# Kernel tuning notes

Measured on AMD Instinct MI355X. Metric: run time of the kernel, lower is better.

Reference implementation:

```python
import jax, jax.numpy as jnp
import numpy as np
import math

# ---------------- real Clebsch-Gordan machinery (numpy, built once at import) ----------------

def _fact(n):
    return math.factorial(n)

def _cg_complex(j1, m1, j2, m2, j3, m3):
    if m1 + m2 != m3:
        return 0.0
    pref = math.sqrt((2 * j3 + 1) * _fact(j3 + j1 - j2) * _fact(j3 - j1 + j2) * _fact(j1 + j2 - j3) / _fact(j1 + j2 + j3 + 1))
    pref *= math.sqrt(_fact(j3 + m3) * _fact(j3 - m3) * _fact(j1 - m1) * _fact(j1 + m1) * _fact(j2 - m2) * _fact(j2 + m2))
    s = 0.0
    for k in range(j1 + j2 - j3 + 1):
        d = [k, j1 + j2 - j3 - k, j1 - m1 - k, j2 + m2 - k, j3 - j2 + m1 + k, j3 - j1 - m2 + k]
        if min(d) < 0:
            continue
        s += (-1) ** k / math.prod(_fact(t) for t in d)
    return pref * s

def _real_U(l):
    # complex -> real spherical-harmonic change of basis, rows = real m (-l..l)
    U = np.zeros((2 * l + 1, 2 * l + 1), dtype=complex)
    U[l, l] = 1.0
    for m in range(1, l + 1):
        U[l + m, l + m] = (-1) ** m / math.sqrt(2)
        U[l + m, l - m] = 1.0 / math.sqrt(2)
        U[l - m, l + m] = -1j * (-1) ** m / math.sqrt(2)
        U[l - m, l - m] = 1j / math.sqrt(2)
    return U

def real_cg(l1, l2, l3):
    C = np.zeros((2 * l1 + 1, 2 * l2 + 1, 2 * l3 + 1), dtype=complex)
    for a in range(-l1, l1 + 1):
        for b in range(-l2, l2 + 1):
            for c in range(-l3, l3 + 1):
                C[a + l1, b + l2, c + l3] = _cg_complex(l1, a, l2, b, l3, c)
    T = np.einsum('ia,jb,kc,abc->ijk', _real_U(l1), _real_U(l2), _real_U(l3).conj(), C)
    Tr, Ti = T.real, T.imag
    T = Tr if np.abs(Tr).sum() >= np.abs(Ti).sum() else Ti
    return (T / np.linalg.norm(T)).astype(np.float32)

# ---------------- irreps / fully-connected tensor product ----------------

IR_SH = [(1, 0, 1), (1, 1, -1), (1, 2, 1), (1, 3, -1)]                      # 1x0e+1x1o+1x2e+1x3o (dim 16)
GATE_IN = [(16, 0, 1), (16, 0, -1), (8, 0, 1), (8, 0, -1), (8, 0, 1), (8, 0, -1), (16, 1, -1), (16, 1, 1)]  # dim 160
GATE_OUT = [(16, 0, 1), (16, 0, -1), (16, 1, -1), (16, 1, 1)]               # dim 128
IR_OUT = [(1, 0, 1)]                                                        # 1x0e

def ir_dim(irs):
    return sum(m * (2 * l + 1) for m, l, _ in irs)

def _slices(irs):
    out, off = [], 0
    for m, l, _ in irs:
        out.append((off, m, 2 * l + 1))
        off += m * (2 * l + 1)
    return out

def make_tp(ir1, ir2, ir3):
    s1, s2, s3 = _slices(ir1), _slices(ir2), _slices(ir3)
    insts, woff = [], 0
    for i1, (m1, l1, p1) in enumerate(ir1):
        for i2, (m2, l2, p2) in enumerate(ir2):
            for i3, (m3, l3, p3) in enumerate(ir3):
                if p1 * p2 == p3 and abs(l1 - l2) <= l3 <= l1 + l2:
                    insts.append((i1, i2, i3, woff))
                    woff += m1 * m2 * m3
    fan = {}
    for i1, i2, i3, _ in insts:
        fan[i3] = fan.get(i3, 0) + ir1[i1][0] * ir2[i2][0]
    paths = []
    for i1, i2, i3, w0 in insts:
        m1, l1, _ = ir1[i1]; m2, l2, _ = ir2[i2]; m3, l3, _ = ir3[i3]
        paths.append(dict(s1=s1[i1], s2=s2[i2], s3=s3[i3], w0=w0, nw=m1 * m2 * m3,
                          cg=jnp.asarray(real_cg(l1, l2, l3)),
                          alpha=math.sqrt((2 * l3 + 1) / fan[i3])))
    return dict(paths=paths, numel=woff, dim_out=ir_dim(ir3))

TP1 = make_tp(IR_SH, IR_SH, GATE_IN)     # weight_numel = 272
TP2 = make_tp(GATE_OUT, IR_SH, IR_OUT)   # weight_numel = 32

def tp_apply(tp, x1, x2, w):
    E = x1.shape[0]
    out = jnp.zeros((E, tp['dim_out']), x1.dtype)
    for p in tp['paths']:
        o1, m1, d1 = p['s1']; o2, m2, d2 = p['s2']; o3, m3, d3 = p['s3']
        a = x1[:, o1:o1 + m1 * d1].reshape(E, m1, d1)
        b = x2[:, o2:o2 + m2 * d2].reshape(E, m2, d2)
        ww = w[:, p['w0']:p['w0'] + p['nw']].reshape(E, m1, m2, m3)
        r = jnp.einsum('eui,evj,euvw,ijk->ewk', a, b, ww, p['cg']) * p['alpha']
        out = out.at[:, o3:o3 + m3 * d3].add(r.reshape(E, m3 * d3))
    return out

# ---------------- spherical harmonics (real, m=-l..l, component normalization) ----------------

SQ3, SQ5, SQ7 = math.sqrt(3), math.sqrt(5), math.sqrt(7)
SQ15, SQ42, SQ70, SQ105 = math.sqrt(15), math.sqrt(42), math.sqrt(70), math.sqrt(105)

def sph_harm_lmax3(v):
    x, y, z = v[:, 0], v[:, 1], v[:, 2]
    x2, y2, z2 = x * x, y * y, z * z
    sh0 = jnp.ones_like(x)[:, None]
    sh1 = SQ3 * jnp.stack([y, z, x], -1)
    sh2 = jnp.stack([SQ15 * x * y, SQ15 * y * z, 0.5 * SQ5 * (3 * z2 - 1), SQ15 * x * z, 0.5 * SQ15 * (x2 - y2)], -1)
    sh3 = jnp.stack([0.25 * SQ70 * y * (3 * x2 - y2), SQ105 * x * y * z, 0.25 * SQ42 * y * (5 * z2 - 1),
                     0.5 * SQ7 * z * (5 * z2 - 3), 0.25 * SQ42 * x * (5 * z2 - 1), 0.5 * SQ105 * z * (x2 - y2),
                     0.25 * SQ70 * x * (x2 - 3 * y2)], -1)
    return jnp.concatenate([sh0, sh1, sh2, sh3], -1)  # [E,16]

MAX_RADIUS, NUM_BASIS = 3.2, 10

def radial_embed(d):
    # soft_one_hot_linspace(basis='smooth_finite', cutoff=True) * sqrt(num_basis)
    step = MAX_RADIUS / (NUM_BASIS + 1)
    centers = jnp.linspace(0.0, MAX_RADIUS, NUM_BASIS + 2)[1:-1]
    u = (d[:, None] - centers) / step
    u2 = u * u
    inner = jnp.where(u2 < 1.0, u2 / jnp.maximum(1.0 - u2, 1e-6), 30.0)
    f = jnp.where(u2 < 1.0, 1.14136 * jnp.exp(-inner), 0.0)
    return f * math.sqrt(NUM_BASIS)

def fcnet(x, w1, w2):
    # e3nn FullyConnectedNet([10, 256, numel], relu): weight/sqrt(fan_in), relu normalized by sqrt(2)
    h = jax.nn.relu(x @ (w1 / math.sqrt(x.shape[1]))) * math.sqrt(2.0)
    return h @ (w2 / math.sqrt(w1.shape[1]))

def gate_act(x):
    # x: [N,160] = 16x0e | 16x0o | 8x0e | 8x0o | 8x0e | 8x0o | 16x1o | 16x1e
    s = jnp.concatenate([jax.nn.relu(x[:, :16]), jnp.tanh(x[:, 16:32])], -1)
    g = jnp.concatenate([jax.nn.relu(x[:, 32:40]), jnp.tanh(x[:, 40:48]),
                         jax.nn.relu(x[:, 48:56]), jnp.tanh(x[:, 56:64])], -1)  # [N,32]
    v = x[:, 64:].reshape(-1, 32, 3)  # 16x1o then 16x1e
    return jnp.concatenate([s, (v * g[:, :, None]).reshape(-1, 96)], -1)  # [N,128]

# ---------------- setup / reference ----------------

def setup_inputs():
    key = jax.random.key(0)
    ks = jax.random.split(key, 8)
    N, E, G = 20000, 640000, 16
    return {
        'pos': jax.random.normal(ks[0], (N, 3), jnp.float32),
        'w_fc1_1': jax.random.normal(ks[1], (NUM_BASIS, 256), jnp.float32),
        'w_fc1_2': jax.random.normal(ks[2], (256, TP1['numel']), jnp.float32),
        'w_fc2_1': jax.random.normal(ks[3], (NUM_BASIS, 256), jnp.float32),
        'w_fc2_2': jax.random.normal(ks[4], (256, TP2['numel']), jnp.float32),
        'edge_src': jax.random.randint(ks[5], (E,), 0, N, jnp.int32),
        'edge_dst': jax.random.randint(ks[6], (E,), 0, N, jnp.int32),
        'batch': jnp.sort(jax.random.randint(ks[7], (N,), 0, G, jnp.int32)),
        'num_graphs': G,
    }

def reference(pos, w_fc1_1, w_fc1_2, w_fc2_1, w_fc2_2, edge_src, edge_dst, batch, num_graphs):
    N = pos.shape[0]
    E = edge_src.shape[0]
    nn_norm = math.sqrt(E / N)  # num_neighbors ** 0.5
    ev = pos[edge_dst] - pos[edge_src]                       # [E,3]
    d = jnp.sqrt(jnp.sum(ev * ev, axis=1) + 1e-12)
    sh = sph_harm_lmax3(ev / d[:, None])                     # [E,16]
    emb = radial_embed(d)                                    # [E,10]
    x = jax.ops.segment_sum(sh, edge_dst, num_segments=N) / nn_norm
    # conv1: per-edge radial MLP -> CG tensor product -> scatter-add
    w = fcnet(emb, w_fc1_1, w_fc1_2)                         # [E,272]
    ef = tp_apply(TP1, x[edge_src], sh, w)                   # [E,160]
    x = jax.ops.segment_sum(ef, edge_dst, num_segments=N) / nn_norm
    x = gate_act(x)                                          # [N,128]
    # conv2
    w = fcnet(emb, w_fc2_1, w_fc2_2)                         # [E,32]
    ef = tp_apply(TP2, x[edge_src], sh, w)                   # [E,1]
    x = jax.ops.segment_sum(ef, edge_dst, num_segments=N) / nn_norm
    return jax.ops.segment_sum(x, batch, num_segments=num_graphs) / math.sqrt(N)  # [G,1]
```

## Files before the change

### kernel.cpp

```cpp
#include <hip/hip_runtime.h>
#include <cmath>
#include <cstdint>
#include <cstring>
#include <cstdlib>
#include <vector>
#include <algorithm>
#include <complex>

#define TILE 32

typedef __attribute__((ext_vector_type(8))) _Float16 f16x8;
typedef __attribute__((ext_vector_type(4))) float f32x4;

struct TPTables {
  uint32_t cg1p[40*10*2];
  uint32_t ovf[64*2];
  int novf;
  uint32_t tabA[12];
  uint32_t tabB[6];
  uint32_t tabC[3];
  uint32_t cg2p[32*4*2];
  uint32_t out2p[32];
  float alpha1[272];
  float alpha2[32];
};

static double factd(int n){ double r=1; for(int i=2;i<=n;i++) r*=(double)i; return r; }

static double cg_complex(int j1,int m1,int j2,int m2,int j3,int m3){
  if(m1+m2!=m3) return 0.0;
  double pref = std::sqrt((2*j3+1)*factd(j3+j1-j2)*factd(j3-j1+j2)*factd(j1+j2-j3)/factd(j1+j2+j3+1));
  pref *= std::sqrt(factd(j3+m3)*factd(j3-m3)*factd(j1-m1)*factd(j1+m1)*factd(j2-m2)*factd(j2+m2));
  double s=0.0;
  for(int k=0;k<=j1+j2-j3;k++){
    int dd[6] = {k, j1+j2-j3-k, j1-m1-k, j2+m2-k, j3-j2+m1+k, j3-j1-m2+k};
    bool ok=true; double prod=1.0;
    for(int t=0;t<6;t++){ if(dd[t]<0){ok=false;break;} prod*=factd(dd[t]); }
    if(!ok) continue;
    s += ((k&1)?-1.0:1.0)/prod;
  }
  return pref*s;
}

typedef std::complex<double> cd;
static void real_U(int l, cd* U){
  int n = 2*l+1;
  for(int i=0;i<n*n;i++) U[i]=cd(0,0);
  U[l*n+l] = cd(1,0);
  for(int m=1;m<=l;m++){
    double sgn = (m&1)? -1.0 : 1.0;
    double is2 = 1.0/std::sqrt(2.0);
    U[(l+m)*n + (l+m)] = cd(sgn*is2,0);
    U[(l+m)*n + (l-m)] = cd(is2,0);
    U[(l-m)*n + (l+m)] = cd(0,-sgn*is2);
    U[(l-m)*n + (l-m)] = cd(0,is2);
  }
}

static void real_cg_h(int l1,int l2,int l3, double* out){
  int n1=2*l1+1,n2=2*l2+1,n3=2*l3+1;
  std::vector<cd> C(n1*n2*n3);
  for(int a=-l1;a<=l1;a++)for(int b=-l2;b<=l2;b++)for(int c=-l3;c<=l3;c++)
    C[(size_t)((a+l1)*n2+(b+l2))*n3+(c+l3)] = cd(cg_complex(l1,a,l2,b,l3,c),0);
  std::vector<cd> U1(n1*n1),U2(n2*n2),U3(n3*n3);
  real_U(l1,U1.data()); real_U(l2,U2.data()); real_U(l3,U3.data());
  std::vector<cd> T((size_t)n1*n2*n3, cd(0,0));
  for(int i=0;i<n1;i++)for(int j=0;j<n2;j++)for(int k=0;k<n3;k++){
    cd acc(0,0);
    for(int a=0;a<n1;a++){ cd u1=U1[i*n1+a]; if(u1==cd(0,0)) continue;
      for(int b=0;b<n2;b++){ cd u2=U2[j*n2+b]; if(u2==cd(0,0)) continue;
        for(int c=0;c<n3;c++){ cd u3=std::conj(U3[k*n3+c]); if(u3==cd(0,0)) continue;
          acc += u1*u2*u3*C[(size_t)(a*n2+b)*n3+c];
        } } }
    T[(size_t)(i*n2+j)*n3+k]=acc;
  }
  double sr=0, si=0;
  for(auto&z:T){ sr += std::fabs(z.real()); si += std::fabs(z.imag()); }
  int tot=n1*n2*n3;
  std::vector<double> R(tot);
  for(int i=0;i<tot;i++) R[i] = (sr>=si)? T[i].real() : T[i].imag();
  double nrm=0; for(double v:R) nrm += v*v; nrm = std::sqrt(nrm);
  for(int i=0;i<tot;i++) out[i] = R[i]/nrm;
}

struct HIrr{int m,l,p;};
static int map_id(int i){return i;}
static int map_gate(int i){return (i<16)? i : i-16;}

static void build_one(const std::vector<HIrr>& ir1, const std::vector<HIrr>& ir2,
                      const std::vector<HIrr>& ir3, int (*map1)(int),
                      std::vector<uint32_t>& cg_pk, std::vector<float>& cg_c,
                      std::vector<uint32_t>& out_pk, std::vector<float>& out_c)
{
  int n1=(int)ir1.size(), n2=(int)ir2.size(), n3=(int)ir3.size();
  std::vector<int> s1(n1), s2(n2), s3(n3);
  { int o=0; for(int i=0;i<n1;i++){ s1[i]=o; o+=ir1[i].m*(2*ir1[i].l+1);} }
  { int o=0; for(int i=0;i<n2;i++){ s2[i]=o; o+=ir2[i].m*(2*ir2[i].l+1);} }
  { int o=0; for(int i=0;i<n3;i++){ s3[i]=o; o+=ir3[i].m*(2*ir3[i].l+1);} }
  struct Inst{int i1,i2,i3,w0;};
  std::vector<Inst> insts; int woff=0;
  for(int i1=0;i1<n1;i1++)for(int i2=0;i2<n2;i2++)for(int i3=0;i3<n3;i3++){
    const HIrr&A=ir1[i1];const HIrr&B=ir2[i2];const HIrr&C=ir3[i3];
    int dl = A.l-B.l; if(dl<0) dl=-dl;
    if(A.p*B.p==C.p && dl<=C.l && C.l<=A.l+B.l){
      insts.push_back({i1,i2,i3,woff}); woff += A.m*B.m*C.m;
    }
  }
  std::vector<int> fan(n3,0);
  for(auto&P:insts) fan[P.i3] += ir1[P.i1].m*ir2[P.i2].m;
  int sbase=0;
  for(auto&P:insts){
    const HIrr&A=ir1[P.i1];const HIrr&B=ir2[P.i2];const HIrr&C=ir3[P.i3];
    int d1=2*A.l+1,d2=2*B.l+1,d3=2*C.l+1;
    double cg[343];
    real_cg_h(A.l,B.l,C.l,cg);
    double alpha = std::sqrt((double)d3/(double)fan[P.i3]);
    for(int u=0;u<A.m;u++)for(int v=0;v<B.m;v++){
      for(int k=0;k<d3;k++)
        for(int i=0;i<d1;i++)for(int j=0;j<d2;j++){
          double c = cg[(i*d2+j)*d3+k];
          if(std::fabs(c)<1e-8) continue;
          int iabs = map1(s1[P.i1]+u*d1+i);
          int jabs = s2[P.i2]+v*d2+j;
          cg_pk.push_back((uint32_t)iabs | ((uint32_t)jabs<<8) | ((uint32_t)(sbase+k)<<16));
          cg_c.push_back((float)c);
        }
      for(int w=0;w<C.m;w++)for(int k=0;k<d3;k++){
        out_pk.push_back((uint32_t)(s3[P.i3]+w*d3+k) | ((uint32_t)(P.w0+(u*B.m+v)*C.m+w)<<8) | ((uint32_t)(sbase+k)<<20));
        out_c.push_back((float)alpha);
      }
      sbase += d3;
    }
  }
}

static uint32_t fbits(float f){ uint32_t u; memcpy(&u,&f,4); return u; }

static void build_tables(TPTables& T){
  std::vector<HIrr> IR_SH   ={{1,0,1},{1,1,-1},{1,2,1},{1,3,-1}};
  std::vector<HIrr> GATE_IN ={{16,0,1},{16,0,-1},{8,0,1},{8,0,-1},{8,0,1},{8,0,-1},{16,1,-1},{16,1,1}};
  std::vector<HIrr> GATE_OUT={{16,0,1},{16,0,-1},{16,1,-1},{16,1,1}};
  std::vector<HIrr> IR_OUT  ={{1,0,1}};
  std::vector<uint32_t> cg1,o1,cg2,o2; std::vector<float> cg1c,o1c,cg2c,o2c;
  build_one(IR_SH,IR_SH,GATE_IN,map_id,cg1,cg1c,o1,o1c);
  build_one(GATE_OUT,IR_SH,IR_OUT,map_gate,cg2,cg2c,o2,o2c);
  memset(&T,0,sizeof(T));
  {
    int cnt[40]; memset(cnt,0,sizeof(cnt));
    for(size_t idx=0; idx<cg1.size(); ++idx){
      int i = cg1[idx]&0xff, j=(cg1[idx]>>8)&0xff, s=(int)(cg1[idx]>>16);
      uint32_t pidx = (uint32_t)(i*16+j);
      if(s<40 && cnt[s]<10){
        T.cg1p[(s*10+cnt[s])*2]   = pidx;
        T.cg1p[(s*10+cnt[s])*2+1] = fbits(cg1c[idx]);
        cnt[s]++;
      } else if(T.novf<64){
        T.ovf[T.novf*2]   = pidx | ((uint32_t)s<<8);
        T.ovf[T.novf*2+1] = fbits(cg1c[idx]);
        T.novf++;
      }
    }
  }
  {
    int GIl[8]={0,0,0,0,0,0,1,1}, GIp[8]={1,-1,1,-1,1,-1,-1,1}, GIm[8]={16,16,8,8,8,8,16,16};
    int SHl[4]={0,1,2,3}, SHp[4]={1,-1,1,-1};
    int w0=0, sb=0, nA0=0,nA1=0,nA2=0,nB=0,nC=0;
    for(int i1=0;i1<4;i1++)for(int i2=0;i2<4;i2++)for(int i3=0;i3<8;i3++){
      int dl=SHl[i1]-SHl[i2]; if(dl<0) dl=-dl;
      if(SHp[i1]*SHp[i2]==GIp[i3] && dl<=GIl[i3] && GIl[i3]<=SHl[i1]+SHl[i2]){
        uint32_t ent = (uint32_t)w0 | ((uint32_t)sb<<16);
        if(i3==0 && nA0<4) T.tabA[nA0++] = ent;
        else if(i3==2 && nA1<4) T.tabA[4+nA1++] = ent;
        else if(i3==4 && nA2<4) T.tabA[8+nA2++] = ent;
        else if(i3==6 && nB<6) T.tabB[nB++] = ent;
        else if(i3==7 && nC<3) T.tabC[nC++] = ent;
        w0 += GIm[i3];
        sb += 2*GIl[i3]+1;
      }
    }
  }
  for(size_t idx=0; idx<o1.size(); ++idx){
    int widx = (o1[idx]>>8)&0xfff;
    if(widx<272) T.alpha1[widx] = o1c[idx];
  }
  {
    int cnt[32]; memset(cnt,0,sizeof(cnt));
    for(size_t idx=0; idx<cg2.size(); ++idx){
      int s = (int)(cg2[idx]>>16);
      if(s<32 && cnt[s]<4){
        T.cg2p[(s*4+cnt[s])*2]   = cg2[idx]&0xFFFF;
        T.cg2p[(s*4+cnt[s])*2+1] = fbits(cg2c[idx]);
        cnt[s]++;
      }
    }
  }
  for(size_t idx=0; idx<o2.size() && idx<32; ++idx){
    int widx = (o2[idx]>>8)&0xfff;
    int s    = (int)(o2[idx]>>20);
    T.out2p[idx] = (uint32_t)widx | ((uint32_t)s<<16);
    if(widx<32) T.alpha2[widx] = o2c[idx];
  }
}

__device__ __forceinline__ unsigned short f2h(float f){
  _Float16 h = (_Float16)f;
  unsigned short u; __builtin_memcpy(&u, &h, 2); return u;
}
__device__ __forceinline__ float h2f(unsigned short u){
  _Float16 h; __builtin_memcpy(&h, &u, 2); return (float)h;
}

__device__ __forceinline__ void sph16(float x,float y,float z,float* sh){
  float x2=x*x, y2=y*y, z2=z*z;
  const float SQ3=1.7320508075688772f, SQ5=2.23606797749979f, SQ7=2.6457513110645907f;
  const float SQ15=3.872983346207417f, SQ42=6.48074069840786f, SQ70=8.366600265340756f, SQ105=10.246950765959598f;
  sh[0]=1.f;
  sh[1]=SQ3*y;  sh[2]=SQ3*z;  sh[3]=SQ3*x;
  sh[4]=SQ15*x*y; sh[5]=SQ15*y*z; sh[6]=0.5f*SQ5*(3.f*z2-1.f); sh[7]=SQ15*x*z; sh[8]=0.5f*SQ15*(x2-y2);
  sh[9]=0.25f*SQ70*y*(3.f*x2-y2); sh[10]=SQ105*x*y*z; sh[11]=0.25f*SQ42*y*(5.f*z2-1.f);
  sh[12]=0.5f*SQ7*z*(5.f*z2-3.f); sh[13]=0.25f*SQ42*x*(5.f*z2-1.f);
  sh[14]=0.5f*SQ105*z*(x2-y2);    sh[15]=0.25f*SQ70*x*(x2-3.f*y2);
}

__device__ __forceinline__ void radial10(float d, float* emb){
  const float step = 0.2909090909090909f;
  #pragma unroll
  for(int b=0;b<10;b++){
    float c = step*(float)(b+1);
    float u = (d-c)/step;
    float u2 = u*u;
    float f = 0.f;
    if(u2<1.f) f = 1.14136f*__expf(-u2/fmaxf(1.f-u2,1e-6f));
    emb[b] = f*3.1622776601683795f;
  }
}

__global__ void k_zero(float* a, size_t na, float* b, size_t nb, float* c, size_t nc,
                       int* d, size_t nd){
  size_t total = na+nb+nc+nd;
  for(size_t i = (size_t)blockIdx.x*blockDim.x+threadIdx.x; i<total; i += (size_t)gridDim.x*blockDim.x){
    if(i<na) a[i]=0.f;
    else if(i<na+nb) b[i-na]=0.f;
    else if(i<na+nb+nc) c[i-na-nb]=0.f;
    else d[i-na-nb-nc]=0;
  }
}

__global__ void k_deg(const int* __restrict__ edst, int* __restrict__ deg, int E){
  int e = blockIdx.x*256 + threadIdx.x;
  if(e<E) atomicAdd(&deg[edst[e]], 1);
}

__global__ __launch_bounds__(1024) void k_scan(const int* __restrict__ deg, int* __restrict__ row,
                                               int* __restrict__ cursor, int N){
  __shared__ int buf[2][1024];
  __shared__ int carry;
  int t = threadIdx.x;
  if(t==0) carry=0;
  __syncthreads();
  for(int base=0; base<N; base+=1024){
    int i = base+t;
    int v = (i<N)? deg[i] : 0;
    int cur=0;
    buf[0][t]=v; __syncthreads();
    for(int off=1; off<1024; off<<=1){
      int val = buf[cur][t];
      if(t>=off) val += buf[cur][t-off];
      buf[cur^1][t]=val; __syncthreads();
      cur^=1;
    }
    if(i<N) row[i] = carry + buf[cur][t] - v;
    int tot = buf[cur][1023];
    __syncthreads();
    if(t==0) carry += tot;
    __syncthreads();
  }
  if(t==0) row[N]=carry;
  for(int i=t;i<N;i+=1024) cursor[i]=0;
}

__global__ void k_fill(const int* __restrict__ edst, const int* __restrict__ row,
                       int* __restrict__ cursor, int* __restrict__ perm, int E){
  int e = blockIdx.x*256 + threadIdx.x;
  if(e<E){
    int d = edst[e];
    int p = atomicAdd(&cursor[d], 1);
    perm[row[d]+p] = e;
  }
}

#define NB1 (17*8*64*8)
#define NB2 (2*8*64*8)
#define NW1 (16*64*8)
__global__ void k_prep(const float* __restrict__ W2a, const float* __restrict__ W2b,
                       const float* __restrict__ W1a, const float* __restrict__ W1b,
                       unsigned short* __restrict__ B1, unsigned short* __restrict__ B2,
                       unsigned short* __restrict__ W1p1, unsigned short* __restrict__ W1p2,
                       const TPTables* __restrict__ T){
  int i = blockIdx.x*256 + threadIdx.x;
  if(i < NB1){
    int s = i&7, lane = (i>>3)&63, ks = (i>>9)&7, ct = i>>12;
    int g = lane>>4;
    int k = ks*32 + g*4 + (s&3) + ((s>>2)<<4);
    int c = ct*16 + (lane&15);
    B1[i] = f2h(W2a[k*272+c]*0.0625f*T->alpha1[c]);
  } else if(i < NB1+NB2){
    int j = i - NB1;
    int s = j&7, lane = (j>>3)&63, ks = (j>>9)&7, ct = j>>12;
    int g = lane>>4;
    int k = ks*32 + g*4 + (s&3) + ((s>>2)<<4);
    int c = ct*16 + (lane&15);
    B2[j] = f2h(W2b[k*32+c]*0.0625f*T->alpha2[c]);
  } else if(i < NB1+NB2+NW1){
    int j = i - NB1 - NB2;
    int s = j&7, lane = (j>>3)&63, ct = j>>9;
    int g = lane>>4;
    int k = g*4 + (s&3) + ((s>>2)<<4);
    int c = ct*16 + (lane&15);
    W1p1[j] = (k<10)? f2h(W1a[k*256+c]*0.4472135954999579f) : (unsigned short)0;
  } else if(i < NB1+NB2+2*NW1){
    int j = i - NB1 - NB2 - NW1;
    int s = j&7, lane = (j>>3)&63, ct = j>>9;
    int g = lane>>4;
    int k = g*4 + (s&3) + ((s>>2)<<4);
    int c = ct*16 + (lane&15);
    W1p2[j] = (k<10)? f2h(W1b[k*256+c]*0.4472135954999579f) : (unsigned short)0;
  }
}

__global__ __launch_bounds__(256) void k_edge_pre(
    const float* __restrict__ pos, const int* __restrict__ esrc, const int* __restrict__ edst,
    const int* __restrict__ perm, float* __restrict__ x, int E){
  __shared__ float shs[256*17];
  __shared__ int dsts[256];
  int t = threadIdx.x;
  int idx = blockIdx.x*256 + t;
  int d = -1;
  if(idx<E){
    int e = perm[idx];
    int s = esrc[e]; d = edst[e];
    float ex=pos[3*d]-pos[3*s], ey=pos[3*d+1]-pos[3*s+1], ez=pos[3*d+2]-pos[3*s+2];
    float dd = sqrtf(ex*ex+ey*ey+ez*ez+1e-12f);
    sph16(ex/dd, ey/dd, ez/dd, &shs[t*17]);
  }
  dsts[t] = d;
  __syncthreads();
  bool leader = (d>=0) && (t==0 || dsts[t-1]!=d);
  if(leader){
    int len=1;
    while(t+len<256 && dsts[t+len]==d) len++;
    #pragma unroll
    for(int j=0;j<16;j++){
      float a=0.f;
      for(int k=0;k<len;k++) a += shs[(t+k)*17+j];
      atomicAdd(&x[(size_t)d*16+j], a);
    }
  }
}

#define F1_WT 1632
#define F1_AF 5984
#define F1_S  10208
#define F1_EF 10848
#define F1_TOT 12928

__global__ __launch_bounds__(512,6) void k_fc1_tp1(
    const float* __restrict__ pos, const int* __restrict__ esrc, const int* __restrict__ edst,
    const int* __restrict__ perm,
    const unsigned short* __restrict__ W1p, const unsigned short* __restrict__ B1,
    const float* __restrict__ xnode, float* __restrict__ ef1,
    const TPTables* __restrict__ T, int E, float inv_nn)
{
  __shared__ __align__(16) float sm[F1_TOT];
  __shared__ int src_t[TILE], dst_t[TILE];
  float* sh_t  = sm;
  float* x1_t  = sm + 544;
  float* emb_t = sm + 1088;
  unsigned short* Wt_h = (unsigned short*)(sm + F1_WT);
  unsigned short* AFh  = (unsigned short*)(sm + F1_AF);
  unsigned short* S16h = (unsigned short*)(sm + F1_S);
  float* ef_h = sm + F1_EF;
  int t = threadIdx.x;
  int e0 = blockIdx.x*TILE;
  int nE = min(TILE, E-e0);
  int e = t>>4, g = t&15, w = t>>6, lane = t&63;
  int g2 = lane>>4, lr = lane&15;

  if(t<TILE){
    float embr[10];
    if(t<nE){
      int e2 = perm[e0+t];
      int s=esrc[e2], d=edst[e2];
      src_t[t]=s; dst_t[t]=d;
      float ex=pos[3*d]-pos[3*s], ey=pos[3*d+1]-pos[3*s+1], ez=pos[3*d+2]-pos[3*s+2];
      float dd=sqrtf(ex*ex+ey*ey+ez*ez+1e-12f);
      sph16(ex/dd,ey/dd,ez/dd, &sh_t[t*17]);
      radial10(dd, embr);
    } else {
      src_t[t]=0; dst_t[t]=-1;
      #pragma unroll
      for(int j=0;j<16;j++) sh_t[t*17+j]=0.f;
      #pragma unroll
      for(int b=0;b<10;b++) embr[b]=0.f;
    }
    #pragma unroll
    for(int b=0;b<10;b++) emb_t[t*17+b]=embr[b];
  }
  __syncthreads();
  x1_t[e*17+g] = xnode[(size_t)src_t[e]*16+g]*inv_nn;
  {
    float af0[8], af1[8];
    #pragma unroll
    for(int s=0;s<8;s++){
      int k = g2*4 + (s&3) + ((s>>2)<<4);
      af0[s] = (k<10)? emb_t[lr*17+k] : 0.f;
      af1[s] = (k<10)? emb_t[(16+lr)*17+k] : 0.f;
    }
    union { f16x8 v; uint32_t w4[4]; } a0u, a1u;
    #pragma unroll
    for(int i=0;i<4;i++){
      a0u.w4[i] = (uint32_t)f2h(af0[2*i]) | ((uint32_t)f2h(af0[2*i+1])<<16);
      a1u.w4[i] = (uint32_t)f2h(af1[2*i]) | ((uint32_t)f2h(af1[2*i+1])<<16);
    }
    #pragma unroll
    for(int q=0;q<2;q++){
      int ct = w*2+q;
      f16x8 b = *(const f16x8*)(W1p + ((size_t)(ct*64+lane))*8);
      f32x4 z = {0.f,0.f,0.f,0.f};
      f32x4 c0 = __builtin_amdgcn_mfma_f32_16x16x32_f16(a0u.v, b, z, 0,0,0);
      f32x4 c1 = __builtin_amdgcn_mfma_f32_16x16x32_f16(a1u.v, b, z, 0,0,0);
      int ks = ct>>1, sp = (lr&3)|((ct&1)<<2);
      #pragma unroll
      for(int r=0;r<4;r++){
        int lnp = ((lr>>2)<<4) + (g2<<2) + r;
        AFh[(ks*64+lnp)*8+sp]     = f2h(fmaxf(c0[r],0.f));
        AFh[((8+ks)*64+lnp)*8+sp] = f2h(fmaxf(c1[r],0.f));
      }
    }
  }
  __syncthreads();
  {
    for(int ct=w; ct<17; ct+=8){
      f32x4 acc0 = {0.f,0.f,0.f,0.f}, acc1 = {0.f,0.f,0.f,0.f};
      #pragma unroll
      for(int ks=0;ks<8;ks++){
        f16x8 b  = *(const f16x8*)(B1 + ((size_t)(ct*8+ks)*64 + lane)*8);
        f16x8 a0 = *(const f16x8*)(AFh + (ks*64+lane)*8);
        f16x8 a1 = *(const f16x8*)(AFh + ((8+ks)*64+lane)*8);
        acc0 = __builtin_amdgcn_mfma_f32_16x16x32_f16(a0, b, acc0, 0,0,0);
        acc1 = __builtin_amdgcn_mfma_f32_16x16x32_f16(a1, b, acc1, 0,0,0);
      }
      #pragma unroll
      for(int r=0;r<4;r++){
        Wt_h[(g2*4+r)*272 + ct*16+lr]    = f2h(acc0[r]);
        Wt_h[(16+g2*4+r)*272 + ct*16+lr] = f2h(acc1[r]);
      }
    }
  }
  __syncthreads();
  {
    float xv = x1_t[e*17+g];
    float shv[16];
    #pragma unroll
    for(int j=0;j<16;j++) shv[j]=sh_t[e*17+j];
    uint32_t* dst = (uint32_t*)AFh + e*132 + g*8;
    #pragma unroll
    for(int jp=0;jp<8;jp++)
      dst[jp] = (uint32_t)f2h(xv*shv[2*jp]) | ((uint32_t)f2h(xv*shv[2*jp+1])<<16);
  }
  __syncthreads();
  {
    const uint2* cgt = (const uint2*)T->cg1p;
    #pragma unroll
    for(int p=0;p<3;p++){
      int slot = p*16+g;
      if(slot<39){
        float acc=0.f;
        #pragma unroll
        for(int q=0;q<10;q++){
          uint2 v = cgt[slot*10+q];
          acc += __uint_as_float(v.y) * h2f(AFh[e*264 + (v.x&0xff)]);
        }
        S16h[e*40+slot] = f2h(acc);
      }
    }
  }
  __syncthreads();
  if(t<TILE){
    int n = T->novf;
    for(int o=0;o<n;o++){
      uint2 v = ((const uint2*)T->ovf)[o];
      int slot = (v.x>>8)&0xff;
      S16h[t*40+slot] = f2h(h2f(S16h[t*40+slot]) + __uint_as_float(v.y)*h2f(AFh[t*264+(v.x&0xff)]));
    }
  }
  __syncthreads();
  float a0=0.f, a1=0.f, accB[3]={0.f,0.f,0.f}, accC[3]={0.f,0.f,0.f};
  {
    int grp = (g>=8)+(g>=12);
    int base = (grp==0)?0:((grp==1)?16:24);
    int ol = g*2 - base;
    #pragma unroll
    for(int p=0;p<4;p++){
      uint32_t v = T->tabA[grp*4+p];
      int w0 = v&0xffff, sb = v>>16;
      float Sv = h2f(S16h[e*40+sb]);
      uint32_t wp = *(const uint32_t*)(Wt_h + e*272 + w0 + ol);
      a0 += h2f((unsigned short)(wp&0xffff))*Sv;
      a1 += h2f((unsigned short)(wp>>16))*Sv;
    }
    #pragma unroll
    for(int p=0;p<6;p++){
      uint32_t v = T->tabB[p];
      int w0 = v&0xffff, sb = v>>16;
      float Wv = h2f(Wt_h[e*272 + w0 + g]);
      accB[0] += Wv*h2f(S16h[e*40+sb]);
      accB[1] += Wv*h2f(S16h[e*40+sb+1]);
      accB[2] += Wv*h2f(S16h[e*40+sb+2]);
    }
    #pragma unroll
    for(int p=0;p<3;p++){
      uint32_t v = T->tabC[p];
      int w0 = v&0xffff, sb = v>>16;
      float Wv = h2f(Wt_h[e*272 + w0 + g]);
      accC[0] += Wv*h2f(S16h[e*40+sb]);
      accC[1] += Wv*h2f(S16h[e*40+sb+1]);
      accC[2] += Wv*h2f(S16h[e*40+sb+2]);
    }
  }
  #pragma unroll
  for(int h=0; h<2; h++){
    for(int i=t;i<TILE*65;i+=512) ef_h[i]=0.f;
    __syncthreads();
    if(h==0){
      ef_h[e*65 + g*2]   = a0;
      ef_h[e*65 + g*2+1] = a1;
      #pragma unroll
      for(int k=0;k<3;k++){
        int b = g*3+k;
        if(b<32) ef_h[e*65 + 32+b] = accB[k];
      }
    } else {
      #pragma unroll
      for(int k=0;k<3;k++){
        int b = g*3+k;
        if(b>=32) ef_h[e*65 + (b-32)] = accB[k];
      }
      #pragma unroll
      for(int k=0;k<3;k++)
        ef_h[e*65 + 16 + g*3+k] = accC[k];
    }
    __syncthreads();
    if(t<64){
      int rank = h*64+t;
      int opos = rank<16? rank : rank<24? rank+16 : rank<32? rank+24 : rank+32;
      float acc=0.f;
      for(int e2=0;e2<TILE;e2++){
        int d = dst_t[e2];
        if(d>=0) acc += ef_h[e2*65+t];
        bool bnd = (e2==TILE-1) || (dst_t[e2+1]!=d);
        if(bnd){
          if(d>=0 && acc!=0.f) atomicAdd(&ef1[(size_t)d*160 + opos], acc);
          acc=0.f;
        }
      }
    }
    __syncthreads();
  }
}

__global__ void k_gate(const float* __restrict__ ef1, float* __restrict__ xg, int N, float inv_nn){
  int n = blockIdx.x*256+threadIdx.x;
  if(n>=N) return;
  const float* v = ef1 + (size_t)n*160;
  float* o = xg + (size_t)n*128;
  float g[32];
  #pragma unroll
  for(int i=0;i<16;i++) o[i] = fmaxf(v[i]*inv_nn, 0.f);
  #pragma unroll
  for(int i=0;i<16;i++) o[16+i] = tanhf(v[16+i]*inv_nn);
  #pragma unroll
  for(int i=0;i<8;i++) g[i]    = fmaxf(v[32+i]*inv_nn,0.f);
  #pragma unroll
  for(int i=0;i<8;i++) g[8+i]  = tanhf(v[40+i]*inv_nn);
  #pragma unroll
  for(int i=0;i<8;i++) g[16+i] = fmaxf(v[48+i]*inv_nn,0.f);
  #pragma unroll
  for(int i=0;i<8;i++) g[24+i] = tanhf(v[56+i]*inv_nn);
  #pragma unroll
  for(int u=0;u<32;u++){
    float gu = g[u];
    #pragma unroll
    for(int k=0;k<3;k++) o[32+u*3+k] = v[64+u*3+k]*inv_nn*gu;
  }
}

#define F2_WT 3168
#define F2_AF 4320
#define F2_BINS 8416
#define F2_TOT 8432

__global__ __launch_bounds__(512,6) void k_fc2_tp2(
    const float* __restrict__ pos, const int* __restrict__ esrc, const int* __restrict__ edst,
    const int* __restrict__ perm, const int* __restrict__ batch,
    const unsigned short* __restrict__ W1p, const unsigned short* __restrict__ B2,
    const float* __restrict__ xg, float* __restrict__ out,
    const TPTables* __restrict__ T, int E, float out_scale, int G)
{
  __shared__ __align__(16) float sm[F2_TOT];
  __shared__ int src_t[TILE], dst_t[TILE], g_t[TILE];
  float* sh_t  = sm;
  float* emb_t = sm + 544;
  float* xg_t  = sm + 1088;
  float* Wt    = sm + F2_WT;
  unsigned short* AFh = (unsigned short*)(sm + F2_AF);
  float* S_l  = sm + F2_AF;
  float* bins = sm + F2_BINS;
  int t = threadIdx.x;
  int e0 = blockIdx.x*TILE;
  int nE = min(TILE, E-e0);
  int e = t>>4, g = t&15, w = t>>6, lane = t&63;
  int g2 = lane>>4, lr = lane&15;

  if(t<TILE){
    float embr[10];
    if(t<nE){
      int e2 = perm[e0+t];
      int s=esrc[e2], d=edst[e2];
      src_t[t]=s; dst_t[t]=d; g_t[t]=batch[d];
      float ex=pos[3*d]-pos[3*s], ey=pos[3*d+1]-pos[3*s+1], ez=pos[3*d+2]-pos[3*s+2];
      float dd=sqrtf(ex*ex+ey*ey+ez*ez+1e-12f);
      sph16(ex/dd,ey/dd,ez/dd, &sh_t[t*17]);
      radial10(dd, embr);
    } else {
      src_t[t]=0; dst_t[t]=-1; g_t[t]=0;
      #pragma unroll
      for(int j=0;j<16;j++) sh_t[t*17+j]=0.f;
      #pragma unroll
      for(int b=0;b<10;b++) embr[b]=0.f;
    }
    #pragma unroll
    for(int b=0;b<10;b++) emb_t[t*17+b]=embr[b];
  } else if(t<TILE+16){
    bins[t-TILE]=0.f;
  }
  __syncthreads();
  #pragma unroll
  for(int rep=0;rep<4;rep++){
    int j = g + rep*16;
    xg_t[e*65+j] = xg[(size_t)src_t[e]*128 + (j<16? j : j+16)];
  }
  {
    float af0[8], af1[8];
    #pragma unroll
    for(int s=0;s<8;s++){
      int k = g2*4 + (s&3) + ((s>>2)<<4);
      af0[s] = (k<10)? emb_t[lr*17+k] : 0.f;
      af1[s] = (k<10)? emb_t[(16+lr)*17+k] : 0.f;
    }
    union { f16x8 v; uint32_t w4[4]; } a0u, a1u;
    #pragma unroll
    for(int i=0;i<4;i++){
      a0u.w4[i] = (uint32_t)f2h(af0[2*i]) | ((uint32_t)f2h(af0[2*i+1])<<16);
      a1u.w4[i] = (uint32_t)f2h(af1[2*i]) | ((uint32_t)f2h(af1[2*i+1])<<16);
    }
    #pragma unroll
    for(int q=0;q<2;q++){
      int ct = w*2+q;
      f16x8 b = *(const f16x8*)(W1p + ((size_t)(ct*64+lane))*8);
      f32x4 z = {0.f,0.f,0.f,0.f};
      f32x4 c0 = __builtin_amdgcn_mfma_f32_16x16x32_f16(a0u.v, b, z, 0,0,0);
      f32x4 c1 = __builtin_amdgcn_mfma_f32_16x16x32_f16(a1u.v, b, z, 0,0,0);
      int ks = ct>>1, sp = (lr&3)|((ct&1)<<2);
      #pragma unroll
      for(int r=0;r<4;r++){
        int lnp = ((lr>>2)<<4) + (g2<<2) + r;
        AFh[(ks*64+lnp)*8+sp]     = f2h(fmaxf(c0[r],0.f));
        AFh[((8+ks)*64+lnp)*8+sp] = f2h(fmaxf(c1[r],0.f));
      }
    }
  }
  __syncthreads();
  {
    if(w<2){
      int ct = w;
      f32x4 acc0 = {0.f,0.f,0.f,0.f}, acc1 = {0.f,0.f,0.f,0.f};
      #pragma unroll
      for(int ks=0;ks<8;ks++){
        f16x8 b  = *(const f16x8*)(B2 + ((size_t)(ct*8+ks)*64 + lane)*8);
        f16x8 a0 = *(const f16x8*)(AFh + (ks*64+lane)*8);
        f16x8 a1 = *(const f16x8*)(AFh + ((8+ks)*64+lane)*8);
        acc0 = __builtin_amdgcn_mfma_f32_16x16x32_f16(a0, b, acc0, 0,0,0);
        acc1 = __builtin_amdgcn_mfma_f32_16x16x32_f16(a1, b, acc1, 0,0,0);
      }
      #pragma unroll
      for(int r=0;r<4;r++){
        Wt[(g2*4+r)*36 + ct*16+lr]    = acc0[r];
        Wt[(16+g2*4+r)*36 + ct*16+lr] = acc1[r];
      }
    }
  }
  __syncthreads();
  {
    const uint2* cgt = (const uint2*)T->cg2p;
    #pragma unroll
    for(int p=0;p<2;p++){
      int slot = p*16 + g;
      float acc=0.f;
      #pragma unroll
      for(int q=0;q<4;q++){
        uint2 v = cgt[slot*4+q];
        acc += __uint_as_float(v.y) * xg_t[e*65+(v.x&0xff)] * sh_t[e*17+((v.x>>8)&0xff)];
      }
      S_l[e*33+slot]=acc;
    }
  }
  __syncthreads();
  {
    uint32_t u0 = T->out2p[2*g], u1 = T->out2p[2*g+1];
    float v = Wt[e*36+(u0&0xffff)] * S_l[e*33+(u0>>16)]
            + Wt[e*36+(u1&0xffff)] * S_l[e*33+(u1>>16)];
    #pragma unroll
    for(int m=1;m<16;m<<=1) v += __shfl_xor(v, m, 64);
    if(g==0 && e<nE) atomicAdd(&bins[g_t[e]], v);
  }
  __syncthreads();
  if(t<G) atomicAdd(&out[t], bins[t]*out_scale);
}

extern "C" void kernel_launch(void* const* d_in, const int* in_sizes, int n_in,
                              void* d_out, int out_size, void* d_ws, size_t ws_size,
                              hipStream_t stream) {
  const float* pos  = (const float*)d_in[0];
  const float* w11  = (const float*)d_in[1];
  const float* w12  = (const float*)d_in[2];
  const float* w21  = (const float*)d_in[3];
  const float* w22  = (const float*)d_in[4];
  const int*   esrc = (const int*)d_in[5];
  const int*   edst = (const int*)d_in[6];
  const int*   batch= (const int*)d_in[7];
  int E = in_sizes[5];
  int N = in_sizes[0]/3;
  int G = out_size;

  double nn = std::sqrt((double)E/(double)N);
  float inv_nn    = (float)(1.0/nn);
  float out_scale = (float)(1.0/(nn*std::sqrt((double)N)));

  float* ws = (float*)d_ws;
  float* x   = ws;
  float* ef1 = x   + (size_t)N*16;
  float* xg  = ef1 + (size_t)N*160;
  TPTables* dT = (TPTables*)(xg + (size_t)N*128);
  unsigned short* B1   = (unsigned short*)(((char*)dT) + ((sizeof(TPTables)+255)&~(size_t)255));
  unsigned short* B2   = B1 + NB1;
  unsigned short* W1p1 = B2 + NB2;
  unsigned short* W1p2 = W1p1 + NW1;
  int* deg    = (int*)(W1p2 + NW1);
  int* row    = deg + N;
  int* cursor = row + (N+1);
  int* perm   = cursor + N;

  static TPTables hT;
  build_tables(hT);
  hipMemcpyAsync(dT, &hT, sizeof(TPTables), hipMemcpyHostToDevice, stream);

  size_t nz = (size_t)N*16 + (size_t)N*160 + G + N;
  int zgrid = (int)((nz+255)/256); if(zgrid>2048) zgrid=2048;
  k_zero<<<zgrid,256,0,stream>>>(x, (size_t)N*16, ef1, (size_t)N*160, (float*)d_out, (size_t)G, deg, (size_t)N);
  k_deg<<<(E+255)/256,256,0,stream>>>(edst, deg, E);
  k_scan<<<1,1024,0,stream>>>(deg, row, cursor, N);
  k_fill<<<(E+255)/256,256,0,stream>>>(edst, row, cursor, perm, E);
  k_prep<<<(NB1+NB2+2*NW1+255)/256,256,0,stream>>>(w12, w22, w11, w21, B1, B2, W1p1, W1p2, dT);
  k_edge_pre<<<(E+255)/256,256,0,stream>>>(pos, esrc, edst, perm, x, E);
  k_fc1_tp1<<<(E+TILE-1)/TILE,512,0,stream>>>(pos, esrc, edst, perm, W1p1, B1, x, ef1, dT, E, inv_nn);
  k_gate<<<(N+255)/256,256,0,stream>>>(ef1, xg, N, inv_nn);
  k_fc2_tp2<<<(E+TILE-1)/TILE,512,0,stream>>>(pos, esrc, edst, perm, batch, W1p2, B2, xg,
                                              (float*)d_out, dT, E, out_scale, G);
}
```

Baseline: 938.3 us.

## Swizzle LDS layouts, pad strides, and drop overflow CG pass in fused kernels

Applies a lane swizzle to the fp16 activation tile written after the first MFMA layer and read by the second, and pads the per-edge weight row strides (272 to 276 halves, 36 to 37 floats) to cut LDS bank conflicts. It widens the per-slot CG table from 10 to 16 entries so every term fits in one pass, which removes the serial overflow loop and a barrier. It also drops the per-half zeroing of the ef buffer and its barrier. The wider CG loop adds some zero-padded multiply-adds, and removing the zeroing assumes every ef entry gets overwritten.

```diff
diff --git a/kernel.cpp b/kernel.cpp
--- a/kernel.cpp
+++ b/kernel.cpp
@@ -13,9 +13,7 @@
 typedef __attribute__((ext_vector_type(4))) float f32x4;
 
 struct TPTables {
-  uint32_t cg1p[40*10*2];
-  uint32_t ovf[64*2];
-  int novf;
+  uint32_t cg1p[40*16*2];
   uint32_t tabA[12];
   uint32_t tabB[6];
   uint32_t tabC[3];
@@ -150,14 +148,10 @@
     for(size_t idx=0; idx<cg1.size(); ++idx){
       int i = cg1[idx]&0xff, j=(cg1[idx]>>8)&0xff, s=(int)(cg1[idx]>>16);
       uint32_t pidx = (uint32_t)(i*16+j);
-      if(s<40 && cnt[s]<10){
-        T.cg1p[(s*10+cnt[s])*2]   = pidx;
-        T.cg1p[(s*10+cnt[s])*2+1] = fbits(cg1c[idx]);
+      if(s<40 && cnt[s]<16){
+        T.cg1p[(s*16+cnt[s])*2]   = pidx;
+        T.cg1p[(s*16+cnt[s])*2+1] = fbits(cg1c[idx]);
         cnt[s]++;
-      } else if(T.novf<64){
-        T.ovf[T.novf*2]   = pidx | ((uint32_t)s<<8);
-        T.ovf[T.novf*2+1] = fbits(cg1c[idx]);
-        T.novf++;
       }
     }
   }
@@ -209,6 +203,7 @@
 __device__ __forceinline__ float h2f(unsigned short u){
   _Float16 h; __builtin_memcpy(&h, &u, 2); return (float)h;
 }
+__device__ __forceinline__ int sig(int x){ return ((x&3)<<4) | (x>>2); }
 
 __device__ __forceinline__ void sph16(float x,float y,float z,float* sh){
   float x2=x*x, y2=y*y, z2=z*z;
@@ -359,10 +354,11 @@
 }
 
 #define F1_WT 1632
-#define F1_AF 5984
-#define F1_S  10208
-#define F1_EF 10848
-#define F1_TOT 12928
+#define F1_AF 6048
+#define F1_S  10272
+#define F1_EF 10912
+#define F1_TOT 12992
+#define WST 276
 
 __global__ __launch_bounds__(512,6) void k_fc1_tp1(
     const float* __restrict__ pos, const int* __restrict__ esrc, const int* __restrict__ edst,
@@ -433,27 +429,29 @@
       #pragma unroll
       for(int r=0;r<4;r++){
         int lnp = ((lr>>2)<<4) + (g2<<2) + r;
-        AFh[(ks*64+lnp)*8+sp]     = f2h(fmaxf(c0[r],0.f));
-        AFh[((8+ks)*64+lnp)*8+sp] = f2h(fmaxf(c1[r],0.f));
-      }
-    }
-  }
-  __syncthreads();
-  {
+        int sl = sig(lnp);
+        AFh[(ks*64+sl)*8+sp]     = f2h(fmaxf(c0[r],0.f));
+        AFh[((8+ks)*64+sl)*8+sp] = f2h(fmaxf(c1[r],0.f));
+      }
+    }
+  }
+  __syncthreads();
+  {
+    int sl = sig(lane);
     for(int ct=w; ct<17; ct+=8){
       f32x4 acc0 = {0.f,0.f,0.f,0.f}, acc1 = {0.f,0.f,0.f,0.f};
       #pragma unroll
       for(int ks=0;ks<8;ks++){
         f16x8 b  = *(const f16x8*)(B1 + ((size_t)(ct*8+ks)*64 + lane)*8);
-        f16x8 a0 = *(const f16x8*)(AFh + (ks*64+lane)*8);
-        f16x8 a1 = *(const f16x8*)(AFh + ((8+ks)*64+lane)*8);
+        f16x8 a0 = *(const f16x8*)(AFh + (ks*64+sl)*8);
+        f16x8 a1 = *(const f16x8*)(AFh + ((8+ks)*64+sl)*8);
         acc0 = __builtin_amdgcn_mfma_f32_16x16x32_f16(a0, b, acc0, 0,0,0);
         acc1 = __builtin_amdgcn_mfma_f32_16x16x32_f16(a1, b, acc1, 0,0,0);
       }
       #pragma unroll
       for(int r=0;r<4;r++){
-        Wt_h[(g2*4+r)*272 + ct*16+lr]    = f2h(acc0[r]);
-        Wt_h[(16+g2*4+r)*272 + ct*16+lr] = f2h(acc1[r]);
+        Wt_h[(g2*4+r)*WST + ct*16+lr]    = f2h(acc0[r]);
+        Wt_h[(16+g2*4+r)*WST + ct*16+lr] = f2h(acc1[r]);
       }
     }
   }
@@ -474,24 +472,15 @@
     #pragma unroll
     for(int p=0;p<3;p++){
       int slot = p*16+g;
-      if(slot<39){
+      if(slot<40){
         float acc=0.f;
         #pragma unroll
-        for(int q=0;q<10;q++){
-          uint2 v = cgt[slot*10+q];
+        for(int q=0;q<16;q++){
+          uint2 v = cgt[slot*16+q];
           acc += __uint_as_float(v.y) * h2f(AFh[e*264 + (v.x&0xff)]);
         }
         S16h[e*40+slot] = f2h(acc);
       }
-    }
-  }
-  __syncthreads();
-  if(t<TILE){
-    int n = T->novf;
-    for(int o=0;o<n;o++){
-      uint2 v = ((const uint2*)T->ovf)[o];
-      int slot = (v.x>>8)&0xff;
-      S16h[t*40+slot] = f2h(h2f(S16h[t*40+slot]) + __uint_as_float(v.y)*h2f(AFh[t*264+(v.x&0xff)]));
     }
   }
   __syncthreads();
@@ -505,7 +494,7 @@
       uint32_t v = T->tabA[grp*4+p];
       int w0 = v&0xffff, sb = v>>16;
       float Sv = h2f(S16h[e*40+sb]);
-      uint32_t wp = *(const uint32_t*)(Wt_h + e*272 + w0 + ol);
+      uint32_t wp = *(const uint32_t*)(Wt_h + e*WST + w0 + ol);
       a0 += h2f((unsigned short)(wp&0xffff))*Sv;
       a1 += h2f((unsigned short)(wp>>16))*Sv;
     }
@@ -513,7 +502,7 @@
     for(int p=0;p<6;p++){
       uint32_t v = T->tabB[p];
       int w0 = v&0xffff, sb = v>>16;
-      float Wv = h2f(Wt_h[e*272 + w0 + g]);
+      float Wv = h2f(Wt_h[e*WST + w0 + g]);
       accB[0] += Wv*h2f(S16h[e*40+sb]);
       accB[1] += Wv*h2f(S16h[e*40+sb+1]);
       accB[2] += Wv*h2f(S16h[e*40+sb+2]);
@@ -522,7 +511,7 @@
     for(int p=0;p<3;p++){
       uint32_t v = T->tabC[p];
       int w0 = v&0xffff, sb = v>>16;
-      float Wv = h2f(Wt_h[e*272 + w0 + g]);
+      float Wv = h2f(Wt_h[e*WST + w0 + g]);
       accC[0] += Wv*h2f(S16h[e*40+sb]);
       accC[1] += Wv*h2f(S16h[e*40+sb+1]);
       accC[2] += Wv*h2f(S16h[e*40+sb+2]);
@@ -530,8 +519,6 @@
   }
   #pragma unroll
   for(int h=0; h<2; h++){
-    for(int i=t;i<TILE*65;i+=512) ef_h[i]=0.f;
-    __syncthreads();
     if(h==0){
       ef_h[e*65 + g*2]   = a0;
       ef_h[e*65 + g*2+1] = a1;
@@ -596,9 +583,9 @@
 }
 
 #define F2_WT 3168
-#define F2_AF 4320
-#define F2_BINS 8416
-#define F2_TOT 8432
+#define F2_AF 4352
+#define F2_BINS 8448
+#define F2_TOT 8464
 
 __global__ __launch_bounds__(512,6) void k_fc2_tp2(
     const float* __restrict__ pos, const int* __restrict__ esrc, const int* __restrict__ edst,
@@ -675,8 +662,9 @@
       #pragma unroll
       for(int r=0;r<4;r++){
         int lnp = ((lr>>2)<<4) + (g2<<2) + r;
-        AFh[(ks*64+lnp)*8+sp]     = f2h(fmaxf(c0[r],0.f));
-        AFh[((8+ks)*64+lnp)*8+sp] = f2h(fmaxf(c1[r],0.f));
+        int sl = sig(lnp);
+        AFh[(ks*64+sl)*8+sp]     = f2h(fmaxf(c0[r],0.f));
+        AFh[((8+ks)*64+sl)*8+sp] = f2h(fmaxf(c1[r],0.f));
       }
     }
   }
@@ -684,19 +672,20 @@
   {
     if(w<2){
       int ct = w;
+      int sl = sig(lane);
       f32x4 acc0 = {0.f,0.f,0.f,0.f}, acc1 = {0.f,0.f,0.f,0.f};
       #pragma unroll
       for(int ks=0;ks<8;ks++){
         f16x8 b  = *(const f16x8*)(B2 + ((size_t)(ct*8+ks)*64 + lane)*8);
-        f16x8 a0 = *(const f16x8*)(AFh + (ks*64+lane)*8);
-        f16x8 a1 = *(const f16x8*)(AFh + ((8+ks)*64+lane)*8);
+        f16x8 a0 = *(const f16x8*)(AFh + (ks*64+sl)*8);
+        f16x8 a1 = *(const f16x8*)(AFh + ((8+ks)*64+sl)*8);
         acc0 = __builtin_amdgcn_mfma_f32_16x16x32_f16(a0, b, acc0, 0,0,0);
         acc1 = __builtin_amdgcn_mfma_f32_16x16x32_f16(a1, b, acc1, 0,0,0);
       }
       #pragma unroll
       for(int r=0;r<4;r++){
-        Wt[(g2*4+r)*36 + ct*16+lr]    = acc0[r];
-        Wt[(16+g2*4+r)*36 + ct*16+lr] = acc1[r];
+        Wt[(g2*4+r)*37 + ct*16+lr]    = acc0[r];
+        Wt[(16+g2*4+r)*37 + ct*16+lr] = acc1[r];
       }
     }
   }
@@ -718,8 +707,8 @@
   __syncthreads();
   {
     uint32_t u0 = T->out2p[2*g], u1 = T->out2p[2*g+1];
-    float v = Wt[e*36+(u0&0xffff)] * S_l[e*33+(u0>>16)]
-            + Wt[e*36+(u1&0xffff)] * S_l[e*33+(u1>>16)];
+    float v = Wt[e*37+(u0&0xffff)] * S_l[e*33+(u0>>16)]
+            + Wt[e*37+(u1&0xffff)] * S_l[e*33+(u1>>16)];
     #pragma unroll
     for(int m=1;m<16;m<<=1) v += __shfl_xor(v, m, 64);
     if(g==0 && e<nE) atomicAdd(&bins[g_t[e]], v);
```

After: 1.140 ms. 21.5% more time.

## Parallelize CSR prefix scan across blocks and swizzle LDS MFMA operand layout

Applied to the files above, without the earlier changes.

Replaces the single-block serial-chunked prefix scan over node degrees with a three-kernel multi-block scan: per-block scans, a wavefront scan of block sums, then an offset add. This removes a long single-workgroup serial loop. It also XOR-swizzles the LDS row index for the hidden-activation fp16 buffer in both fc+TP kernels to reduce bank conflicts on stores and MFMA operand loads. The scan handles at most 64 blocks (N up to 65536) and adds two extra launches.

```diff
diff --git a/kernel.cpp b/kernel.cpp
--- a/kernel.cpp
+++ b/kernel.cpp
@@ -209,6 +209,7 @@
 __device__ __forceinline__ float h2f(unsigned short u){
   _Float16 h; __builtin_memcpy(&h, &u, 2); return (float)h;
 }
+__device__ __forceinline__ int sig(int x){ return x ^ (x>>3); }
 
 __device__ __forceinline__ void sph16(float x,float y,float z,float* sh){
   float x2=x*x, y2=y*y, z2=z*z;
@@ -251,32 +252,42 @@
   if(e<E) atomicAdd(&deg[edst[e]], 1);
 }
 
-__global__ __launch_bounds__(1024) void k_scan(const int* __restrict__ deg, int* __restrict__ row,
-                                               int* __restrict__ cursor, int N){
+__global__ __launch_bounds__(1024) void k_scan1(const int* __restrict__ deg, int* __restrict__ row,
+                                                int* __restrict__ bsum, int N){
   __shared__ int buf[2][1024];
-  __shared__ int carry;
   int t = threadIdx.x;
-  if(t==0) carry=0;
-  __syncthreads();
-  for(int base=0; base<N; base+=1024){
-    int i = base+t;
-    int v = (i<N)? deg[i] : 0;
-    int cur=0;
-    buf[0][t]=v; __syncthreads();
-    for(int off=1; off<1024; off<<=1){
-      int val = buf[cur][t];
-      if(t>=off) val += buf[cur][t-off];
-      buf[cur^1][t]=val; __syncthreads();
-      cur^=1;
-    }
-    if(i<N) row[i] = carry + buf[cur][t] - v;
-    int tot = buf[cur][1023];
-    __syncthreads();
-    if(t==0) carry += tot;
-    __syncthreads();
-  }
-  if(t==0) row[N]=carry;
-  for(int i=t;i<N;i+=1024) cursor[i]=0;
+  int i = blockIdx.x*1024 + t;
+  int v = (i<N)? deg[i] : 0;
+  int cur=0;
+  buf[0][t]=v; __syncthreads();
+  for(int off=1; off<1024; off<<=1){
+    int val = buf[cur][t];
+    if(t>=off) val += buf[cur][t-off];
+    buf[cur^1][t]=val; __syncthreads();
+    cur^=1;
+  }
+  if(i<N) row[i] = buf[cur][t] - v;
+  if(t==1023) bsum[blockIdx.x] = buf[cur][t];
+}
+__global__ void k_scan2(int* __restrict__ bsum, int nb){
+  int t = threadIdx.x;
+  int v = (t<nb)? bsum[t] : 0;
+  #pragma unroll
+  for(int off=1; off<64; off<<=1){
+    int u = __shfl_up(v, off, 64);
+    if(t>=off) v += u;
+  }
+  if(t<nb) bsum[t] = v;
+}
+__global__ void k_scan3(int* __restrict__ row, const int* __restrict__ bsum,
+                        int* __restrict__ cursor, int N, int nb){
+  int i = blockIdx.x*256 + threadIdx.x;
+  if(i<N){
+    int b = i>>10;
+    if(b>0) row[i] += bsum[b-1];
+    cursor[i]=0;
+  }
+  if(i==0) row[N] = bsum[nb-1];
 }
 
 __global__ void k_fill(const int* __restrict__ edst, const int* __restrict__ row,
@@ -433,20 +444,22 @@
       #pragma unroll
       for(int r=0;r<4;r++){
         int lnp = ((lr>>2)<<4) + (g2<<2) + r;
-        AFh[(ks*64+lnp)*8+sp]     = f2h(fmaxf(c0[r],0.f));
-        AFh[((8+ks)*64+lnp)*8+sp] = f2h(fmaxf(c1[r],0.f));
-      }
-    }
-  }
-  __syncthreads();
-  {
+        int sl = sig(lnp);
+        AFh[(ks*64+sl)*8+sp]     = f2h(fmaxf(c0[r],0.f));
+        AFh[((8+ks)*64+sl)*8+sp] = f2h(fmaxf(c1[r],0.f));
+      }
+    }
+  }
+  __syncthreads();
+  {
+    int sl = sig(lane);
     for(int ct=w; ct<17; ct+=8){
       f32x4 acc0 = {0.f,0.f,0.f,0.f}, acc1 = {0.f,0.f,0.f,0.f};
       #pragma unroll
       for(int ks=0;ks<8;ks++){
         f16x8 b  = *(const f16x8*)(B1 + ((size_t)(ct*8+ks)*64 + lane)*8);
-        f16x8 a0 = *(const f16x8*)(AFh + (ks*64+lane)*8);
-        f16x8 a1 = *(const f16x8*)(AFh + ((8+ks)*64+lane)*8);
+        f16x8 a0 = *(const f16x8*)(AFh + (ks*64+sl)*8);
+        f16x8 a1 = *(const f16x8*)(AFh + ((8+ks)*64+sl)*8);
         acc0 = __builtin_amdgcn_mfma_f32_16x16x32_f16(a0, b, acc0, 0,0,0);
         acc1 = __builtin_amdgcn_mfma_f32_16x16x32_f16(a1, b, acc1, 0,0,0);
       }
@@ -675,8 +688,9 @@
       #pragma unroll
       for(int r=0;r<4;r++){
         int lnp = ((lr>>2)<<4) + (g2<<2) + r;
-        AFh[(ks*64+lnp)*8+sp]     = f2h(fmaxf(c0[r],0.f));
-        AFh[((8+ks)*64+lnp)*8+sp] = f2h(fmaxf(c1[r],0.f));
+        int sl = sig(lnp);
+        AFh[(ks*64+sl)*8+sp]     = f2h(fmaxf(c0[r],0.f));
+        AFh[((8+ks)*64+sl)*8+sp] = f2h(fmaxf(c1[r],0.f));
       }
     }
   }
@@ -684,12 +698,13 @@
   {
     if(w<2){
       int ct = w;
+      int sl = sig(lane);
       f32x4 acc0 = {0.f,0.f,0.f,0.f}, acc1 = {0.f,0.f,0.f,0.f};
       #pragma unroll
       for(int ks=0;ks<8;ks++){
         f16x8 b  = *(const f16x8*)(B2 + ((size_t)(ct*8+ks)*64 + lane)*8);
-        f16x8 a0 = *(const f16x8*)(AFh + (ks*64+lane)*8);
-        f16x8 a1 = *(const f16x8*)(AFh + ((8+ks)*64+lane)*8);
+        f16x8 a0 = *(const f16x8*)(AFh + (ks*64+sl)*8);
+        f16x8 a1 = *(const f16x8*)(AFh + ((8+ks)*64+sl)*8);
         acc0 = __builtin_amdgcn_mfma_f32_16x16x32_f16(a0, b, acc0, 0,0,0);
         acc1 = __builtin_amdgcn_mfma_f32_16x16x32_f16(a1, b, acc1, 0,0,0);
       }
@@ -760,16 +775,20 @@
   int* row    = deg + N;
   int* cursor = row + (N+1);
   int* perm   = cursor + N;
+  int* bsum   = perm + E;
 
   static TPTables hT;
   build_tables(hT);
   hipMemcpyAsync(dT, &hT, sizeof(TPTables), hipMemcpyHostToDevice, stream);
 
+  int nb = (N+1023)/1024;
   size_t nz = (size_t)N*16 + (size_t)N*160 + G + N;
   int zgrid = (int)((nz+255)/256); if(zgrid>2048) zgrid=2048;
   k_zero<<<zgrid,256,0,stream>>>(x, (size_t)N*16, ef1, (size_t)N*160, (float*)d_out, (size_t)G, deg, (size_t)N);
   k_deg<<<(E+255)/256,256,0,stream>>>(edst, deg, E);
-  k_scan<<<1,1024,0,stream>>>(deg, row, cursor, N);
+  k_scan1<<<nb,1024,0,stream>>>(deg, row, bsum, N);
+  k_scan2<<<1,64,0,stream>>>(bsum, nb);
+  k_scan3<<<(N+255)/256,256,0,stream>>>(row, bsum, cursor, N, nb);
   k_fill<<<(E+255)/256,256,0,stream>>>(edst, row, cursor, perm, E);
   k_prep<<<(NB1+NB2+2*NW1+255)/256,256,0,stream>>>(w12, w22, w11, w21, B1, B2, W1p1, W1p2, dT);
   k_edge_pre<<<(E+255)/256,256,0,stream>>>(pos, esrc, edst, perm, x, E);
```

New measurement: 905.8 us. 1.04x faster.
